# Optimization experiments

Hardware: AMD Instinct MI355X
Metric: run time of the kernel (lower is better)

## Reference

```python
import jax, jax.numpy as jnp
import numpy as np

B, L, H, W = 4, 16, 4096, 128   # W == nfeat == nclass (required by out.reshape)
NHID = 256

def setup_inputs() -> dict:
    key = jax.random.key(0)
    k1, k2, k3, k4 = jax.random.split(key, 4)
    x = jax.random.normal(k1, (B, L, H, W), dtype=jnp.float32)
    # row-normalized-ish dense adjacency stand-in for the sparse normalized adj
    adj = jax.random.uniform(k2, (H, H), dtype=jnp.float32) / H
    # GraphConvolution params: support = input @ Wk; out = adj @ support + bk
    W1 = jax.random.normal(k3, (W, NHID), dtype=jnp.float32) / np.sqrt(W)
    b1 = jnp.zeros((NHID,), dtype=jnp.float32)
    W2 = jax.random.normal(k4, (NHID, W), dtype=jnp.float32) / np.sqrt(NHID)
    b2 = jnp.zeros((W,), dtype=jnp.float32)
    return {"x": x, "adj": adj, "W1": W1, "b1": b1, "W2": W2, "b2": b2}

def reference(x, adj, W1, b1, W2, b2):
    Bv, Lv, Hv, Wv = x.shape
    xf = x.reshape(Bv * Lv, Hv, Wv)                      # [BL, H, F]
    # gc1: transform then aggregate, fused over all slices (replaces per-slice loop)
    h = jnp.einsum('nm,bmf->bnf', adj, xf @ W1) + b1     # [BL, H, nhid]
    h = jax.nn.relu(h)
    # dropout: inference mode (training=False) -> identity
    out = jnp.einsum('nm,bmf->bnf', adj, h @ W2) + b2    # [BL, H, nclass]
    out = out.reshape(Bv, Lv, Hv, Wv)
    return jax.nn.log_softmax(out, axis=-1)
```

## Files before the change

### kernel.cpp

```cpp
#include <hip/hip_runtime.h>

typedef __attribute__((ext_vector_type(4))) float f32x4;
typedef __attribute__((ext_vector_type(16))) float f32x16;
typedef __attribute__((ext_vector_type(4))) int i32x4;
typedef __attribute__((ext_vector_type(8))) int i32x8;
typedef union { i32x8 v8; i32x4 v4[2]; } opnd;

__device__ __forceinline__ unsigned fp4q(float v) {
  float a = __builtin_fabsf(v);
  unsigned q = (unsigned)(a > 0.25f) + (a > 0.75f) + (a > 1.25f) + (a > 1.75f)
             + (a > 2.5f) + (a > 3.5f) + (a > 5.0f);
  return q | (v < 0.0f ? 8u : 0u);
}

#if __has_builtin(__builtin_amdgcn_cvt_scalef32_pk_fp4_f32)
#define PKFP4(old, x, y, s) __builtin_amdgcn_cvt_scalef32_pk_fp4_f32((old), (x), (y), 1.0f, (s))
#else
#define PKFP4(old, x, y, s) ((old) | ((fp4q(x) | (fp4q(y) << 4)) << (8 * (s))))
#endif

__device__ __forceinline__ long tiled_addr(long r, long k, int nkb) {
  return (((r >> 5) * nkb) + (k >> 6)) * 2048 + ((k & 16) ? 1024 : 0)
       + (((r & 31) + (((k >> 5) & 1) << 5)) << 4) + (k & 15);
}
__device__ __forceinline__ long tile4_addr(long r, long k, int nkb) {
  return (((r >> 5) * nkb) + (k >> 6)) * 1024
       + (((r & 31) + (((k >> 5) & 1) << 5)) << 4) + ((k & 31) >> 1);
}

__device__ __forceinline__ long remap_wg(int lin, int nwg, int gx) {
  long g = lin;
  if ((nwg & 7) == 0) {
    int cpx = nwg >> 3;
    int gyx = cpx / gx;
    int xcd = lin & 7, idx = lin >> 3;
    if ((gx & 3) == 0 && gyx >= 4 && (gyx & 3) == 0) {
      int st = idx >> 4, wi = idx & 15;
      int nstr = gx >> 2;
      int str = st % nstr, stc = st / nstr;
      int r = str * 4 + (wi & 3);
      int c2 = stc * 4 + (wi >> 2);
      g = (long)xcd * cpx + (long)c2 * gx + r;
    } else {
      g = (long)xcd * cpx + idx;
    }
  }
  return g;
}

__global__ __launch_bounds__(256) void cvtAdj4t(const float* __restrict__ in,
                                                unsigned char* __restrict__ out, long n) {
  long i = ((long)blockIdx.x * 256 + threadIdx.x) * 8;
  if (i >= n) return;
  float4 a = *(const float4*)(in + i);
  float4 b = *(const float4*)(in + i + 4);
  const float S = 24576.0f;
  unsigned word = PKFP4(0u, a.x * S, a.y * S, 0);
  word = PKFP4(word, a.z * S, a.w * S, 1);
  word = PKFP4(word, b.x * S, b.y * S, 2);
  word = PKFP4(word, b.z * S, b.w * S, 3);
  long r = i >> 12;
  long k = i & 4095;
  *(int*)(out + tile4_addr(r, k, 64)) = (int)word;
}

__global__ __launch_bounds__(256) void cvtX4t(const float* __restrict__ X,
                                              unsigned char* __restrict__ out4) {
  __shared__ float tile[32][33];
  const int tid = threadIdx.x;
  const long bl = blockIdx.z;
  const int m0 = blockIdx.y * 32;
  const int w0 = blockIdx.x * 32;
  const float* xb = X + (bl * 4096 + m0) * 128 + w0;
  int row = tid >> 3, cg = tid & 7;
  float4 v = *(const float4*)(xb + (long)row * 128 + cg * 4);
  tile[row][cg * 4 + 0] = v.x;
  tile[row][cg * 4 + 1] = v.y;
  tile[row][cg * 4 + 2] = v.z;
  tile[row][cg * 4 + 3] = v.w;
  __syncthreads();
  if (tid < 128) {
    int wv = tid & 31, mg = tid >> 5;
    float t[8];
#pragma unroll
    for (int i = 0; i < 8; ++i) t[i] = tile[mg * 8 + i][wv];
    unsigned word = PKFP4(0u, t[0], t[1], 0);
    word = PKFP4(word, t[2], t[3], 1);
    word = PKFP4(word, t[4], t[5], 2);
    word = PKFP4(word, t[6], t[7], 3);
    long r = bl * 128 + w0 + wv;
    long k = m0 + mg * 8;
    *(int*)(out4 + tile4_addr(r, k, 64)) = (int)word;
  }
}

__global__ __launch_bounds__(256) void prep_params(const float* __restrict__ W1,
                                                   const float* __restrict__ W2,
                                                   unsigned char* __restrict__ W1T8,
                                                   unsigned char* __restrict__ W2T8) {
  int idx = blockIdx.x * 256 + threadIdx.x;
  if (idx < 32768) {
    int f = idx >> 7, wv = idx & 127;
    float v = W1[wv * 256 + f] * 16.0f;
    int pk = __builtin_amdgcn_cvt_pk_fp8_f32(v, v, 0, 0);
    W1T8[tiled_addr(f, wv, 2)] = (unsigned char)(pk & 0xff);
  } else {
    int t = idx - 32768;
    int cc = t >> 8, f = t & 255;
    float v = W2[f * 128 + cc] * 16.0f;
    int pk = __builtin_amdgcn_cvt_pk_fp8_f32(v, v, 0, 0);
    W2T8[tiled_addr(cc, f, 4)] = (unsigned char)(pk & 0xff);
  }
}

__global__ __launch_bounds__(256, 3) void gemmS1(const unsigned char* __restrict__ A4,
                                                 const unsigned char* __restrict__ X4,
                                                 const unsigned char* __restrict__ W1T8,
                                                 const unsigned char* __restrict__ W2T8,
                                                 unsigned char* __restrict__ t2T4,
                                                 const float* __restrict__ b1,
                                                 int K, int gx) {
  __shared__ unsigned char lds[49152];
  const int tid = threadIdx.x;
  const int l = tid & 63;
  const int w = tid >> 6;
  long g = remap_wg(blockIdx.x, gridDim.x, gx);
  const long row0 = (g % gx) * 128;
  const long bl = g / gx;
  const int nkb = K >> 6;
  const int wr = w >> 1, wc = w & 1;
  const unsigned char* sAp = A4 + (((row0 >> 5) + w) * (long)nkb) * 1024 + l * 16;
  const unsigned char* sXp = X4 + ((bl * 4 + w) * (long)nkb) * 1024 + l * 16;
  unsigned char* ldsw = lds + w * 1024;
  const unsigned char* rA = lds + (wr * 2) * 1024 + l * 16;
  const unsigned char* rX = lds + 4096 + (wc * 2) * 1024 + l * 16;

  f32x16 acc[2][2] = {};
  opnd aE[2], xE[2], aO[2], xO[2];
  const i32x4 z4 = {0, 0, 0, 0};
#pragma unroll
  for (int fi = 0; fi < 2; ++fi) {
    aE[fi].v4[1] = z4; xE[fi].v4[1] = z4;
    aO[fi].v4[1] = z4; xO[fi].v4[1] = z4;
  }

#define STG(B, SL) do { long o0_ = (long)(2 * (B)) * 1024; long o1_ = o0_ + 1024;     \
    unsigned char* d_ = ldsw + (SL) * 16384;                                          \
    __builtin_amdgcn_global_load_lds((const unsigned int*)(const void*)(sAp + o0_),   \
                                     (unsigned int*)(d_), 16, 0, 0);                  \
    __builtin_amdgcn_global_load_lds((const unsigned int*)(const void*)(sXp + o0_),   \
                                     (unsigned int*)(d_ + 4096), 16, 0, 0);           \
    __builtin_amdgcn_global_load_lds((const unsigned int*)(const void*)(sAp + o1_),   \
                                     (unsigned int*)(d_ + 8192), 16, 0, 0);           \
    __builtin_amdgcn_global_load_lds((const unsigned int*)(const void*)(sXp + o1_),   \
                                     (unsigned int*)(d_ + 12288), 16, 0, 0);          \
  } while (0)
#define LDF(SL, HALF, AV, XV) do { const long s_ = (SL) * 16384 + (HALF) * 8192;      \
    AV[0].v4[0] = *(const i32x4*)(rA + s_);                                           \
    AV[1].v4[0] = *(const i32x4*)(rA + s_ + 1024);                                    \
    XV[0].v4[0] = *(const i32x4*)(rX + s_);                                           \
    XV[1].v4[0] = *(const i32x4*)(rX + s_ + 1024); } while (0)
#define MFMAS(AV, XV) do {                                                            \
    __builtin_amdgcn_s_setprio(1);                                                    \
    _Pragma("unroll") for (int fi = 0; fi < 2; ++fi)                                  \
      _Pragma("unroll") for (int j = 0; j < 2; ++j)                                   \
        acc[fi][j] = __builtin_amdgcn_mfma_scale_f32_32x32x64_f8f6f4(                 \
            XV[j].v8, AV[fi].v8, acc[fi][j], 4, 4, 0, 127, 0, 124);                   \
    __builtin_amdgcn_s_setprio(0); } while (0)
#define BODY(SL, SS, DOSTG, B, N) do {                                                \
    LDF(SL, 0, aE, xE);                                                               \
    if (DOSTG) STG((B) + 2, SS);                                                      \
    LDF(SL, 1, aO, xO);                                                               \
    MFMAS(aE, xE);                                                                    \
    MFMAS(aO, xO);                                                                    \
    asm volatile("s_waitcnt vmcnt(" N ")" ::: "memory");                              \
    __builtin_amdgcn_s_barrier(); } while (0)

  STG(0, 0); STG(1, 1);
  asm volatile("s_waitcnt vmcnt(4)" ::: "memory");
  __builtin_amdgcn_s_barrier();
  for (int b = 0; b < 30; b += 3) {
    BODY(0, 2, 1, b + 0, "4");
    BODY(1, 0, 1, b + 1, "4");
    BODY(2, 1, 1, b + 2, "4");
  }
  BODY(0, 0, 0, 30, "0");
  BODY(1, 0, 0, 31, "0");
#undef STG
#undef LDF
#undef MFMAS
#undef BODY

  unsigned char* S1buf = lds;
  unsigned char* hbuf = lds + 16384;

  const int hi = l >> 5;
  const int ln = l & 31;
#pragma unroll
  for (int fi = 0; fi < 2; ++fi) {
    int n = (wr * 2 + fi) * 32 + ln;
#pragma unroll
    for (int j = 0; j < 2; ++j) {
      int wb = (wc * 2 + j) * 32 + 4 * hi;
#pragma unroll
      for (int r4 = 0; r4 < 4; ++r4) {
        int w0 = wb + 8 * r4;
        int word = __builtin_amdgcn_cvt_pk_fp8_f32(acc[fi][j][4 * r4 + 0],
                                                   acc[fi][j][4 * r4 + 1], 0, false);
        word = __builtin_amdgcn_cvt_pk_fp8_f32(acc[fi][j][4 * r4 + 2],
                                               acc[fi][j][4 * r4 + 3], word, true);
        *(int*)(S1buf + tiled_addr(n, w0, 2)) = word;
      }
    }
  }
  __syncthreads();

  const float c1 = 128.0f / 49152.0f;
#pragma unroll
  for (int hh = 0; hh < 2; ++hh) {
#pragma unroll
    for (int fi = 0; fi < 2; ++fi)
#pragma unroll
      for (int jb = 0; jb < 2; ++jb) acc[fi][jb] = (f32x16){};
#pragma unroll
    for (int kt1 = 0; kt1 < 2; ++kt1) {
#pragma unroll
      for (int jb = 0; jb < 2; ++jb) {
        opnd aw;
        const unsigned char* pW = W1T8 + (long)((hh * 4 + wc * 2 + jb) * 2 + kt1) * 2048 + l * 16;
        aw.v4[0] = *(const i32x4*)(pW);
        aw.v4[1] = *(const i32x4*)(pW + 1024);
#pragma unroll
        for (int fi = 0; fi < 2; ++fi) {
          opnd bs;
          const unsigned char* pS = S1buf + (long)((wr * 2 + fi) * 2 + kt1) * 2048 + l * 16;
          bs.v4[0] = *(const i32x4*)(pS);
          bs.v4[1] = *(const i32x4*)(pS + 1024);
          acc[fi][jb] = __builtin_amdgcn_mfma_scale_f32_32x32x64_f8f6f4(
              aw.v8, bs.v8, acc[fi][jb], 0, 0, 0, 127, 0, 127);
        }
      }
    }
#pragma unroll
    for (int jb = 0; jb < 2; ++jb) {
      int fb = (hh * 4 + wc * 2 + jb) * 32 + 4 * hi;
#pragma unroll
      for (int r4 = 0; r4 < 4; ++r4) {
        int f0 = fb + 8 * r4;
        float4 bb = *(const float4*)(b1 + f0);
#pragma unroll
        for (int fi = 0; fi < 2; ++fi) {
          int n = (wr * 2 + fi) * 32 + ln;
          float v0 = fmaxf(fmaf(acc[fi][jb][4 * r4 + 0], c1, bb.x * 128.0f), 0.0f);
          float v1 = fmaxf(fmaf(acc[fi][jb][4 * r4 + 1], c1, bb.y * 128.0f), 0.0f);
          float v2 = fmaxf(fmaf(acc[fi][jb][4 * r4 + 2], c1, bb.z * 128.0f), 0.0f);
          float v3 = fmaxf(fmaf(acc[fi][jb][4 * r4 + 3], c1, bb.w * 128.0f), 0.0f);
          int word = __builtin_amdgcn_cvt_pk_fp8_f32(v0, v1, 0, false);
          word = __builtin_amdgcn_cvt_pk_fp8_f32(v2, v3, word, true);
          *(int*)(hbuf + tiled_addr(n, f0, 4)) = word;
        }
      }
    }
  }
  __syncthreads();

#pragma unroll
  for (int fi = 0; fi < 2; ++fi)
#pragma unroll
    for (int jb = 0; jb < 2; ++jb) acc[fi][jb] = (f32x16){};
#pragma unroll
  for (int kt2 = 0; kt2 < 4; ++kt2) {
#pragma unroll
    for (int jb = 0; jb < 2; ++jb) {
      opnd bw;
      const unsigned char* pW = W2T8 + (long)((wc * 2 + jb) * 4 + kt2) * 2048 + l * 16;
      bw.v4[0] = *(const i32x4*)(pW);
      bw.v4[1] = *(const i32x4*)(pW + 1024);
#pragma unroll
      for (int fi = 0; fi < 2; ++fi) {
        opnd ah;
        const unsigned char* pH = hbuf + (long)((wr * 2 + fi) * 4 + kt2) * 2048 + l * 16;
        ah.v4[0] = *(const i32x4*)(pH);
        ah.v4[1] = *(const i32x4*)(pH + 1024);
        acc[fi][jb] = __builtin_amdgcn_mfma_scale_f32_32x32x64_f8f6f4(
            ah.v8, bw.v8, acc[fi][jb], 0, 0, 0, 127, 0, 127);
      }
    }
  }
  unsigned char* ob = t2T4 + bl * 262144;
#pragma unroll
  for (int fi = 0; fi < 2; ++fi) {
#pragma unroll
    for (int jb = 0; jb < 2; ++jb) {
      int cc = wc * 64 + jb * 32 + ln;
#pragma unroll
      for (int run = 0; run < 4; ++run) {
        long n0 = row0 + wr * 64 + fi * 32 + 8 * run + 4 * hi;
        const float s = 0.125f;
        unsigned pkw = PKFP4(0u, acc[fi][jb][run * 4 + 0] * s,
                                 acc[fi][jb][run * 4 + 1] * s, 0);
        pkw = PKFP4(pkw, acc[fi][jb][run * 4 + 2] * s,
                         acc[fi][jb][run * 4 + 3] * s, 1);
        *(ushort*)(ob + tile4_addr(cc, n0, 64)) = (ushort)pkw;
      }
    }
  }
}

__global__ __launch_bounds__(512) void gemm256sm(const unsigned char* __restrict__ A4,
                                                 const unsigned char* __restrict__ B4,
                                                 float* __restrict__ out,
                                                 const float* __restrict__ bias,
                                                 float ooScale, int K, int gx,
                                                 int chunkBase) {
  __shared__ unsigned char ring[65536];
  const int tid = threadIdx.x;
  const int l = tid & 63;
  const int w = tid >> 6;
  int lin = blockIdx.x;
  const int nwg = gridDim.x;
  if (gx == 16 && (nwg & 63) == 0) {
    int xcd = lin & 7, idx = lin >> 3;
    int cpg = nwg >> 6;
    int r = ((xcd & 1) << 3) + (idx & 7);
    int c = (xcd >> 1) * cpg + (idx >> 3);
    lin = c * gx + r;
  } else if ((nwg & 7) == 0) {
    int cpx = nwg >> 3;
    lin = (lin & 7) * cpx + (lin >> 3);
  }
  const long row0 = (long)(lin % gx) * 256;
  const long col0 = (long)(lin / gx) * 256;
  const int nkb = K >> 6;
  const unsigned char* sBp = B4 + (((col0 >> 5) + w) * (long)nkb) * 1024 + l * 16;
  unsigned char* ringw = ring + w * 1024;
  const unsigned char* ringr = ring + ((w & 1) * 4) * 1024 + l * 16;
  const unsigned char* pA = A4 + (((row0 + (w >> 1) * 64) >> 5) * (long)nkb) * 1024 + l * 16;

  f32x16 acc[2][4] = {};
  opnd bv[4], a0v[2], a1v[2], a2v[2], a3v[2];
  const i32x4 z4 = {0, 0, 0, 0};
#pragma unroll
  for (int j = 0; j < 4; ++j) bv[j].v4[1] = z4;
#pragma unroll
  for (int fi = 0; fi < 2; ++fi) {
    a0v[fi].v4[1] = z4; a1v[fi].v4[1] = z4; a2v[fi].v4[1] = z4; a3v[fi].v4[1] = z4;
  }

#define STGB(KT) __builtin_amdgcn_global_load_lds(                                    \
    (const unsigned int*)(const void*)(sBp + (long)(KT) * 1024),                      \
    (unsigned int*)(ringw + (((KT) & 7) << 13)), 16, 0, 0)
#define LOADA(KT, AV) do { long o_ = (long)(KT) * 1024;                               \
    AV[0].v4[0] = *(const i32x4*)(pA + o_);                                           \
    AV[1].v4[0] = *(const i32x4*)(pA + (long)nkb * 1024 + o_); } while (0)
#define LDB(KT) do { const unsigned char* p_ = ringr + (((KT) & 7) << 13);            \
    bv[0].v4[0] = *(const i32x4*)(p_);                                                \
    bv[1].v4[0] = *(const i32x4*)(p_ + 1024);                                         \
    bv[2].v4[0] = *(const i32x4*)(p_ + 2048);                                         \
    bv[3].v4[0] = *(const i32x4*)(p_ + 3072); } while (0)
#define MFMAS(AV) do { __builtin_amdgcn_s_setprio(1);                                 \
    _Pragma("unroll") for (int fi = 0; fi < 2; ++fi)                                  \
      _Pragma("unroll") for (int j = 0; j < 4; ++j)                                   \
        acc[fi][j] = __builtin_amdgcn_mfma_scale_f32_32x32x64_f8f6f4(                 \
            AV[fi].v8, bv[j].v8, acc[fi][j], 4, 4, 0, 127, 0, 127);                   \
    __builtin_amdgcn_s_setprio(0); } while (0)
#define BODY(KT, N, DOSTG, DOA, ALD, AUSE) do {                                       \
    LDB(KT);                                                                          \
    if (DOA) LOADA((KT) + 3, ALD);                                                    \
    if (DOSTG) STGB((KT) + 6);                                                        \
    asm volatile("s_waitcnt vmcnt(" N ")" ::: "memory");                              \
    MFMAS(AUSE);                                                                      \
    __builtin_amdgcn_s_barrier(); } while (0)

  const int nkt = K >> 6;
  LOADA(0, a0v); LOADA(1, a1v); LOADA(2, a2v);
  STGB(0); STGB(1); STGB(2); STGB(3); STGB(4); STGB(5);
  asm volatile("s_waitcnt vmcnt(5)" ::: "memory");
  __builtin_amdgcn_s_barrier();

  BODY(0, "7", 1, 1, a3v, a0v);
  BODY(1, "9", 1, 1, a0v, a1v);
  BODY(2, "11", 1, 1, a1v, a2v);
  for (int kt = 3; kt + 9 <= nkt - 1; kt += 4) {
    BODY(kt,     "10", 1, 1, a2v, a3v);
    BODY(kt + 1, "10", 1, 1, a3v, a0v);
    BODY(kt + 2, "10", 1, 1, a0v, a1v);
    BODY(kt + 3, "10", 1, 1, a1v, a2v);
  }
  BODY(55, "10", 1, 1, a2v, a3v);
  BODY(56, "10", 1, 1, a3v, a0v);
  BODY(57, "10", 1, 1, a0v, a1v);
  BODY(58, "9",  0, 1, a1v, a2v);
  BODY(59, "8",  0, 1, a2v, a3v);
  BODY(60, "7",  0, 1, a3v, a0v);
  BODY(61, "4",  0, 0, a0v, a1v);
  BODY(62, "2",  0, 0, a0v, a2v);
  BODY(63, "0",  0, 0, a0v, a3v);
#undef STGB
#undef LOADA
#undef LDB
#undef MFMAS
#undef BODY

  const int hi = l >> 5;
  const int bl = (int)(col0 >> 7) + (w & 1);
  float bb[4];
#pragma unroll
  for (int j = 0; j < 4; ++j) bb[j] = bias[j * 32 + (l & 31)];
#pragma unroll
  for (int fi = 0; fi < 2; ++fi) {
#pragma unroll
    for (int rr = 0; rr < 16; ++rr) {
      float v0 = acc[fi][0][rr] * ooScale + bb[0];
      float v1 = acc[fi][1][rr] * ooScale + bb[1];
      float v2 = acc[fi][2][rr] * ooScale + bb[2];
      float v3 = acc[fi][3][rr] * ooScale + bb[3];
      float m = fmaxf(fmaxf(v0, v1), fmaxf(v2, v3));
#pragma unroll
      for (int o = 16; o > 0; o >>= 1) m = fmaxf(m, __shfl_xor(m, o));
      float s = __expf(v0 - m) + __expf(v1 - m) + __expf(v2 - m) + __expf(v3 - m);
#pragma unroll
      for (int o = 16; o > 0; o >>= 1) s += __shfl_xor(s, o);
      float lse = m + __logf(s);
      long row = row0 + (w >> 1) * 64 + fi * 32 + ((rr & 3) + 8 * (rr >> 2) + 4 * hi);
      float* dst = out + ((long)(chunkBase + bl) * 4096 + row) * 128;
      dst[(l & 31)] = v0 - lse;
      dst[32 + (l & 31)] = v1 - lse;
      dst[64 + (l & 31)] = v2 - lse;
      dst[96 + (l & 31)] = v3 - lse;
    }
  }
}

extern "C" void kernel_launch(void* const* d_in, const int* in_sizes, int n_in,
                              void* d_out, int out_size, void* d_ws, size_t ws_size,
                              hipStream_t stream) {
  const float* x = (const float*)d_in[0];
  const float* adj = (const float*)d_in[1];
  const float* W1 = (const float*)d_in[2];
  const float* b1 = (const float*)d_in[3];
  const float* W2 = (const float*)d_in[4];
  const float* b2 = (const float*)d_in[5];
  float* out = (float*)d_out;
  char* ws = (char*)d_ws;

  unsigned char* adj4 = (unsigned char*)ws;
  unsigned char* W1T8 = (unsigned char*)(ws + 8388608);
  unsigned char* W2T8 = (unsigned char*)(ws + 8388608 + 32768);
  const size_t base = 9ull * 1024 * 1024;

  const int cands[6] = {64, 32, 16, 8, 4, 2};
  int c = 2;
  for (int t = 0; t < 6; ++t) {
    size_t need = base + (size_t)cands[t] * 524288;
    if (need <= ws_size) { c = cands[t]; break; }
  }
  unsigned char* x4T = (unsigned char*)(ws + base);
  unsigned char* t2T4 = x4T + (size_t)c * 262144;

  cvtAdj4t<<<8192, 256, 0, stream>>>(adj, adj4, (long)4096 * 4096);
  prep_params<<<256, 256, 0, stream>>>(W1, W2, W1T8, W2T8);

  int chunks = 64 / c;
  for (int cb = 0; cb < chunks; ++cb) {
    int base_bl = cb * c;
    const float* xc = x + (long)base_bl * 4096 * 128;

    cvtX4t<<<dim3(4, 128, c), 256, 0, stream>>>(xc, x4T);
    gemmS1<<<32 * c, 256, 0, stream>>>(adj4, x4T, W1T8, W2T8, t2T4, b1, 4096, 32);
    gemm256sm<<<16 * (c / 2), 512, 0, stream>>>(adj4, t2T4, out, b2,
                                                1.0f / 6291456.0f, 4096, 16, base_bl);
  }
}
```

Before: 229.9 us.

## Split MFMA loop bodies into ping-pong phases with barrier-synced LDS loads

Both GEMM main loops are split into two half-phases. Each phase issues its LDS fragment loads, meets a workgroup barrier, waits on lgkmcnt, and then runs half of the MFMAs behind a sched_barrier. The aim is to interleave waves so memory and matrix work alternate across the workgroup, ping-pong style. The second kernel's vmcnt thresholds are loosened so more global loads stay in flight. The cost is extra barriers per iteration, and the hand-tuned vmcnt counts carry a correctness risk if they are miscounted.

```diff
diff --git a/kernel.cpp b/kernel.cpp
--- a/kernel.cpp
+++ b/kernel.cpp
@@ -167,29 +167,40 @@
         acc[fi][j] = __builtin_amdgcn_mfma_scale_f32_32x32x64_f8f6f4(                 \
             XV[j].v8, AV[fi].v8, acc[fi][j], 4, 4, 0, 127, 0, 124);                   \
     __builtin_amdgcn_s_setprio(0); } while (0)
-#define BODY(SL, SS, DOSTG, B, N) do {                                                \
+#define PH1S(SL, SS, DOSTG, B) do {                                                   \
     LDF(SL, 0, aE, xE);                                                               \
     if (DOSTG) STG((B) + 2, SS);                                                      \
+    __builtin_amdgcn_s_barrier();                                                     \
+    asm volatile("s_waitcnt lgkmcnt(0)" ::: "memory");                                \
+    __builtin_amdgcn_sched_barrier(0);                                                \
+    MFMAS(aE, xE);                                                                    \
+    __builtin_amdgcn_s_barrier(); } while (0)
+#define PH2S(SL, N) do {                                                              \
     LDF(SL, 1, aO, xO);                                                               \
-    MFMAS(aE, xE);                                                                    \
+    __builtin_amdgcn_s_barrier();                                                     \
+    asm volatile("s_waitcnt lgkmcnt(0)" ::: "memory");                                \
+    __builtin_amdgcn_sched_barrier(0);                                                \
     MFMAS(aO, xO);                                                                    \
     asm volatile("s_waitcnt vmcnt(" N ")" ::: "memory");                              \
     __builtin_amdgcn_s_barrier(); } while (0)
+#define BODYS(SL, SS, DOSTG, B, N) do { PH1S(SL, SS, DOSTG, B); PH2S(SL, N); } while (0)
 
   STG(0, 0); STG(1, 1);
   asm volatile("s_waitcnt vmcnt(4)" ::: "memory");
   __builtin_amdgcn_s_barrier();
   for (int b = 0; b < 30; b += 3) {
-    BODY(0, 2, 1, b + 0, "4");
-    BODY(1, 0, 1, b + 1, "4");
-    BODY(2, 1, 1, b + 2, "4");
-  }
-  BODY(0, 0, 0, 30, "0");
-  BODY(1, 0, 0, 31, "0");
+    BODYS(0, 2, 1, b + 0, "4");
+    BODYS(1, 0, 1, b + 1, "4");
+    BODYS(2, 1, 1, b + 2, "4");
+  }
+  BODYS(0, 0, 0, 30, "0");
+  BODYS(1, 0, 0, 31, "0");
 #undef STG
 #undef LDF
 #undef MFMAS
-#undef BODY
+#undef PH1S
+#undef PH2S
+#undef BODYS
 
   unsigned char* S1buf = lds;
   unsigned char* hbuf = lds + 16384;
@@ -353,23 +364,39 @@
 #define LOADA(KT, AV) do { long o_ = (long)(KT) * 1024;                               \
     AV[0].v4[0] = *(const i32x4*)(pA + o_);                                           \
     AV[1].v4[0] = *(const i32x4*)(pA + (long)nkb * 1024 + o_); } while (0)
-#define LDB(KT) do { const unsigned char* p_ = ringr + (((KT) & 7) << 13);            \
+#define LDB01(KT) do { const unsigned char* p_ = ringr + (((KT) & 7) << 13);          \
     bv[0].v4[0] = *(const i32x4*)(p_);                                                \
-    bv[1].v4[0] = *(const i32x4*)(p_ + 1024);                                         \
+    bv[1].v4[0] = *(const i32x4*)(p_ + 1024); } while (0)
+#define LDB23(KT) do { const unsigned char* p_ = ringr + (((KT) & 7) << 13);          \
     bv[2].v4[0] = *(const i32x4*)(p_ + 2048);                                         \
     bv[3].v4[0] = *(const i32x4*)(p_ + 3072); } while (0)
-#define MFMAS(AV) do { __builtin_amdgcn_s_setprio(1);                                 \
+#define MFMA01(AV) do { __builtin_amdgcn_s_setprio(1);                                \
     _Pragma("unroll") for (int fi = 0; fi < 2; ++fi)                                  \
-      _Pragma("unroll") for (int j = 0; j < 4; ++j)                                   \
+      _Pragma("unroll") for (int j = 0; j < 2; ++j)                                   \
+        acc[fi][j] = __builtin_amdgcn_mfma_scale_f32_32x32x64_f8f6f4(                 \
+            AV[fi].v8, bv[j].v8, acc[fi][j], 4, 4, 0, 127, 0, 127);                   \
+    __builtin_amdgcn_s_setprio(0); } while (0)
+#define MFMA23(AV) do { __builtin_amdgcn_s_setprio(1);                                \
+    _Pragma("unroll") for (int fi = 0; fi < 2; ++fi)                                  \
+      _Pragma("unroll") for (int j = 2; j < 4; ++j)                                   \
         acc[fi][j] = __builtin_amdgcn_mfma_scale_f32_32x32x64_f8f6f4(                 \
             AV[fi].v8, bv[j].v8, acc[fi][j], 4, 4, 0, 127, 0, 127);                   \
     __builtin_amdgcn_s_setprio(0); } while (0)
 #define BODY(KT, N, DOSTG, DOA, ALD, AUSE) do {                                       \
-    LDB(KT);                                                                          \
+    LDB01(KT);                                                                        \
+    if (DOSTG) STGB((KT) + 6);                                                        \
+    __builtin_amdgcn_s_barrier();                                                     \
+    asm volatile("s_waitcnt lgkmcnt(0)" ::: "memory");                                \
+    __builtin_amdgcn_sched_barrier(0);                                                \
+    MFMA01(AUSE);                                                                     \
+    __builtin_amdgcn_s_barrier();                                                     \
+    LDB23(KT);                                                                        \
     if (DOA) LOADA((KT) + 3, ALD);                                                    \
-    if (DOSTG) STGB((KT) + 6);                                                        \
+    __builtin_amdgcn_s_barrier();                                                     \
+    asm volatile("s_waitcnt lgkmcnt(0)" ::: "memory");                                \
+    __builtin_amdgcn_sched_barrier(0);                                                \
+    MFMA23(AUSE);                                                                     \
     asm volatile("s_waitcnt vmcnt(" N ")" ::: "memory");                              \
-    MFMAS(AUSE);                                                                      \
     __builtin_amdgcn_s_barrier(); } while (0)
 
   const int nkt = K >> 6;
@@ -378,28 +405,34 @@
   asm volatile("s_waitcnt vmcnt(5)" ::: "memory");
   __builtin_amdgcn_s_barrier();
 
-  BODY(0, "7", 1, 1, a3v, a0v);
-  BODY(1, "9", 1, 1, a0v, a1v);
+  BODY(0, "7",  1, 1, a3v, a0v);
+  BODY(1, "9",  1, 1, a0v, a1v);
   BODY(2, "11", 1, 1, a1v, a2v);
-  for (int kt = 3; kt + 9 <= nkt - 1; kt += 4) {
-    BODY(kt,     "10", 1, 1, a2v, a3v);
-    BODY(kt + 1, "10", 1, 1, a3v, a0v);
-    BODY(kt + 2, "10", 1, 1, a0v, a1v);
-    BODY(kt + 3, "10", 1, 1, a1v, a2v);
-  }
-  BODY(55, "10", 1, 1, a2v, a3v);
-  BODY(56, "10", 1, 1, a3v, a0v);
-  BODY(57, "10", 1, 1, a0v, a1v);
-  BODY(58, "9",  0, 1, a1v, a2v);
-  BODY(59, "8",  0, 1, a2v, a3v);
-  BODY(60, "7",  0, 1, a3v, a0v);
-  BODY(61, "4",  0, 0, a0v, a1v);
-  BODY(62, "2",  0, 0, a0v, a2v);
+  BODY(3, "13", 1, 1, a2v, a3v);
+  BODY(4, "15", 1, 1, a3v, a0v);
+  for (int kt = 5; kt <= 49; kt += 4) {
+    BODY(kt,     "17", 1, 1, a0v, a1v);
+    BODY(kt + 1, "17", 1, 1, a1v, a2v);
+    BODY(kt + 2, "17", 1, 1, a2v, a3v);
+    BODY(kt + 3, "17", 1, 1, a3v, a0v);
+  }
+  BODY(53, "17", 1, 1, a0v, a1v);
+  BODY(54, "17", 1, 1, a1v, a2v);
+  BODY(55, "17", 1, 1, a2v, a3v);
+  BODY(56, "17", 1, 1, a3v, a0v);
+  BODY(57, "17", 1, 1, a0v, a1v);
+  BODY(58, "16", 0, 1, a1v, a2v);
+  BODY(59, "15", 0, 1, a2v, a3v);
+  BODY(60, "14", 0, 1, a3v, a0v);
+  BODY(61, "11", 0, 0, a0v, a1v);
+  BODY(62, "8",  0, 0, a0v, a2v);
   BODY(63, "0",  0, 0, a0v, a3v);
 #undef STGB
 #undef LOADA
-#undef LDB
-#undef MFMAS
+#undef LDB01
+#undef LDB23
+#undef MFMA01
+#undef MFMA23
 #undef BODY
 
   const int hi = l >> 5;
```

Result: no change. 233.1 us (+1.4%).

## Retile second adjacency GEMM into 128-row, 256-thread blocks with shared staging pipeline

Applied to the files above, without the earlier changes.

Replaces the 256x256, 512-thread second-stage GEMM with a 128-row x one-slice tile using 256 threads. It reuses the triple-buffered LDS staging scheme from the first GEMM, which loads both A and B via global_load_lds. The launch grid changes to 32 blocks per slice with occupancy hint of 3 blocks per CU. This aims at more parallelism and a simpler pipeline, at the cost of less operand reuse per block and more total adjacency traffic.

```diff
diff --git a/kernel.cpp b/kernel.cpp
--- a/kernel.cpp
+++ b/kernel.cpp
@@ -167,7 +167,7 @@
         acc[fi][j] = __builtin_amdgcn_mfma_scale_f32_32x32x64_f8f6f4(                 \
             XV[j].v8, AV[fi].v8, acc[fi][j], 4, 4, 0, 127, 0, 124);                   \
     __builtin_amdgcn_s_setprio(0); } while (0)
-#define BODY(SL, SS, DOSTG, B, N) do {                                                \
+#define BODYS(SL, SS, DOSTG, B, N) do {                                               \
     LDF(SL, 0, aE, xE);                                                               \
     if (DOSTG) STG((B) + 2, SS);                                                      \
     LDF(SL, 1, aO, xO);                                                               \
@@ -180,16 +180,16 @@
   asm volatile("s_waitcnt vmcnt(4)" ::: "memory");
   __builtin_amdgcn_s_barrier();
   for (int b = 0; b < 30; b += 3) {
-    BODY(0, 2, 1, b + 0, "4");
-    BODY(1, 0, 1, b + 1, "4");
-    BODY(2, 1, 1, b + 2, "4");
-  }
-  BODY(0, 0, 0, 30, "0");
-  BODY(1, 0, 0, 31, "0");
+    BODYS(0, 2, 1, b + 0, "4");
+    BODYS(1, 0, 1, b + 1, "4");
+    BODYS(2, 1, 1, b + 2, "4");
+  }
+  BODYS(0, 0, 0, 30, "0");
+  BODYS(1, 0, 0, 31, "0");
 #undef STG
 #undef LDF
 #undef MFMAS
-#undef BODY
+#undef BODYS
 
   unsigned char* S1buf = lds;
   unsigned char* hbuf = lds + 16384;
@@ -307,128 +307,103 @@
   }
 }
 
-__global__ __launch_bounds__(512) void gemm256sm(const unsigned char* __restrict__ A4,
-                                                 const unsigned char* __restrict__ B4,
-                                                 float* __restrict__ out,
-                                                 const float* __restrict__ bias,
-                                                 float ooScale, int K, int gx,
-                                                 int chunkBase) {
-  __shared__ unsigned char ring[65536];
+__global__ __launch_bounds__(256, 3) void gemm256sm(const unsigned char* __restrict__ A4,
+                                                    const unsigned char* __restrict__ B4,
+                                                    float* __restrict__ out,
+                                                    const float* __restrict__ bias,
+                                                    float ooScale, int K, int gx,
+                                                    int chunkBase) {
+  __shared__ unsigned char lds[49152];
   const int tid = threadIdx.x;
   const int l = tid & 63;
   const int w = tid >> 6;
-  int lin = blockIdx.x;
-  const int nwg = gridDim.x;
-  if (gx == 16 && (nwg & 63) == 0) {
-    int xcd = lin & 7, idx = lin >> 3;
-    int cpg = nwg >> 6;
-    int r = ((xcd & 1) << 3) + (idx & 7);
-    int c = (xcd >> 1) * cpg + (idx >> 3);
-    lin = c * gx + r;
-  } else if ((nwg & 7) == 0) {
-    int cpx = nwg >> 3;
-    lin = (lin & 7) * cpx + (lin >> 3);
-  }
-  const long row0 = (long)(lin % gx) * 256;
-  const long col0 = (long)(lin / gx) * 256;
+  long g = remap_wg(blockIdx.x, gridDim.x, gx);
+  const long row0 = (g % gx) * 128;
+  const long bl = g / gx;
   const int nkb = K >> 6;
-  const unsigned char* sBp = B4 + (((col0 >> 5) + w) * (long)nkb) * 1024 + l * 16;
-  unsigned char* ringw = ring + w * 1024;
-  const unsigned char* ringr = ring + ((w & 1) * 4) * 1024 + l * 16;
-  const unsigned char* pA = A4 + (((row0 + (w >> 1) * 64) >> 5) * (long)nkb) * 1024 + l * 16;
-
-  f32x16 acc[2][4] = {};
-  opnd bv[4], a0v[2], a1v[2], a2v[2], a3v[2];
+  const unsigned char* sAp = A4 + (((row0 >> 5) + w) * (long)nkb) * 1024 + l * 16;
+  const unsigned char* sXp = B4 + ((bl * 4 + w) * (long)nkb) * 1024 + l * 16;
+  unsigned char* ldsw = lds + w * 1024;
+  const unsigned char* rA = lds + w * 1024 + l * 16;
+  const unsigned char* rB = lds + 4096 + l * 16;
+
+  f32x16 acc[4] = {};
+  opnd aE, aO, bE[4], bO[4];
   const i32x4 z4 = {0, 0, 0, 0};
-#pragma unroll
-  for (int j = 0; j < 4; ++j) bv[j].v4[1] = z4;
-#pragma unroll
-  for (int fi = 0; fi < 2; ++fi) {
-    a0v[fi].v4[1] = z4; a1v[fi].v4[1] = z4; a2v[fi].v4[1] = z4; a3v[fi].v4[1] = z4;
-  }
-
-#define STGB(KT) __builtin_amdgcn_global_load_lds(                                    \
-    (const unsigned int*)(const void*)(sBp + (long)(KT) * 1024),                      \
-    (unsigned int*)(ringw + (((KT) & 7) << 13)), 16, 0, 0)
-#define LOADA(KT, AV) do { long o_ = (long)(KT) * 1024;                               \
-    AV[0].v4[0] = *(const i32x4*)(pA + o_);                                           \
-    AV[1].v4[0] = *(const i32x4*)(pA + (long)nkb * 1024 + o_); } while (0)
-#define LDB(KT) do { const unsigned char* p_ = ringr + (((KT) & 7) << 13);            \
-    bv[0].v4[0] = *(const i32x4*)(p_);                                                \
-    bv[1].v4[0] = *(const i32x4*)(p_ + 1024);                                         \
-    bv[2].v4[0] = *(const i32x4*)(p_ + 2048);                                         \
-    bv[3].v4[0] = *(const i32x4*)(p_ + 3072); } while (0)
-#define MFMAS(AV) do { __builtin_amdgcn_s_setprio(1);                                 \
-    _Pragma("unroll") for (int fi = 0; fi < 2; ++fi)                                  \
-      _Pragma("unroll") for (int j = 0; j < 4; ++j)                                   \
-        acc[fi][j] = __builtin_amdgcn_mfma_scale_f32_32x32x64_f8f6f4(                 \
-            AV[fi].v8, bv[j].v8, acc[fi][j], 4, 4, 0, 127, 0, 127);                   \
+  aE.v4[1] = z4; aO.v4[1] = z4;
+#pragma unroll
+  for (int j = 0; j < 4; ++j) { bE[j].v4[1] = z4; bO[j].v4[1] = z4; }
+
+#define STG(B, SL) do { long o0_ = (long)(2 * (B)) * 1024; long o1_ = o0_ + 1024;     \
+    unsigned char* d_ = ldsw + (SL) * 16384;                                          \
+    __builtin_amdgcn_global_load_lds((const unsigned int*)(const void*)(sAp + o0_),   \
+                                     (unsigned int*)(d_), 16, 0, 0);                  \
+    __builtin_amdgcn_global_load_lds((const unsigned int*)(const void*)(sXp + o0_),   \
+                                     (unsigned int*)(d_ + 4096), 16, 0, 0);           \
+    __builtin_amdgcn_global_load_lds((const unsigned int*)(const void*)(sAp + o1_),   \
+                                     (unsigned int*)(d_ + 8192), 16, 0, 0);           \
+    __builtin_amdgcn_global_load_lds((const unsigned int*)(const void*)(sXp + o1_),   \
+                                     (unsigned int*)(d_ + 12288), 16, 0, 0);          \
+  } while (0)
+#define LDF(SL, HALF, AV, BV) do { const long s_ = (SL) * 16384 + (HALF) * 8192;      \
+    AV.v4[0] = *(const i32x4*)(rA + s_);                                              \
+    BV[0].v4[0] = *(const i32x4*)(rB + s_);                                           \
+    BV[1].v4[0] = *(const i32x4*)(rB + s_ + 1024);                                    \
+    BV[2].v4[0] = *(const i32x4*)(rB + s_ + 2048);                                    \
+    BV[3].v4[0] = *(const i32x4*)(rB + s_ + 3072); } while (0)
+#define MFMAS(AV, BV) do {                                                            \
+    __builtin_amdgcn_s_setprio(1);                                                    \
+    _Pragma("unroll") for (int j = 0; j < 4; ++j)                                     \
+      acc[j] = __builtin_amdgcn_mfma_scale_f32_32x32x64_f8f6f4(                       \
+          AV.v8, BV[j].v8, acc[j], 4, 4, 0, 127, 0, 127);                             \
     __builtin_amdgcn_s_setprio(0); } while (0)
-#define BODY(KT, N, DOSTG, DOA, ALD, AUSE) do {                                       \
-    LDB(KT);                                                                          \
-    if (DOA) LOADA((KT) + 3, ALD);                                                    \
-    if (DOSTG) STGB((KT) + 6);                                                        \
+#define BODYS(SL, SS, DOSTG, B, N) do {                                               \
+    LDF(SL, 0, aE, bE);                                                               \
+    if (DOSTG) STG((B) + 2, SS);                                                      \
+    LDF(SL, 1, aO, bO);                                                               \
+    MFMAS(aE, bE);                                                                    \
+    MFMAS(aO, bO);                                                                    \
     asm volatile("s_waitcnt vmcnt(" N ")" ::: "memory");                              \
-    MFMAS(AUSE);                                                                      \
     __builtin_amdgcn_s_barrier(); } while (0)
 
-  const int nkt = K >> 6;
-  LOADA(0, a0v); LOADA(1, a1v); LOADA(2, a2v);
-  STGB(0); STGB(1); STGB(2); STGB(3); STGB(4); STGB(5);
-  asm volatile("s_waitcnt vmcnt(5)" ::: "memory");
+  STG(0, 0); STG(1, 1);
+  asm volatile("s_waitcnt vmcnt(4)" ::: "memory");
   __builtin_amdgcn_s_barrier();
-
-  BODY(0, "7", 1, 1, a3v, a0v);
-  BODY(1, "9", 1, 1, a0v, a1v);
-  BODY(2, "11", 1, 1, a1v, a2v);
-  for (int kt = 3; kt + 9 <= nkt - 1; kt += 4) {
-    BODY(kt,     "10", 1, 1, a2v, a3v);
-    BODY(kt + 1, "10", 1, 1, a3v, a0v);
-    BODY(kt + 2, "10", 1, 1, a0v, a1v);
-    BODY(kt + 3, "10", 1, 1, a1v, a2v);
-  }
-  BODY(55, "10", 1, 1, a2v, a3v);
-  BODY(56, "10", 1, 1, a3v, a0v);
-  BODY(57, "10", 1, 1, a0v, a1v);
-  BODY(58, "9",  0, 1, a1v, a2v);
-  BODY(59, "8",  0, 1, a2v, a3v);
-  BODY(60, "7",  0, 1, a3v, a0v);
-  BODY(61, "4",  0, 0, a0v, a1v);
-  BODY(62, "2",  0, 0, a0v, a2v);
-  BODY(63, "0",  0, 0, a0v, a3v);
-#undef STGB
-#undef LOADA
-#undef LDB
+  for (int b = 0; b < 30; b += 3) {
+    BODYS(0, 2, 1, b + 0, "4");
+    BODYS(1, 0, 1, b + 1, "4");
+    BODYS(2, 1, 1, b + 2, "4");
+  }
+  BODYS(0, 0, 0, 30, "0");
+  BODYS(1, 0, 0, 31, "0");
+#undef STG
+#undef LDF
 #undef MFMAS
-#undef BODY
+#undef BODYS
 
   const int hi = l >> 5;
-  const int bl = (int)(col0 >> 7) + (w & 1);
   float bb[4];
 #pragma unroll
   for (int j = 0; j < 4; ++j) bb[j] = bias[j * 32 + (l & 31)];
 #pragma unroll
-  for (int fi = 0; fi < 2; ++fi) {
-#pragma unroll
-    for (int rr = 0; rr < 16; ++rr) {
-      float v0 = acc[fi][0][rr] * ooScale + bb[0];
-      float v1 = acc[fi][1][rr] * ooScale + bb[1];
-      float v2 = acc[fi][2][rr] * ooScale + bb[2];
-      float v3 = acc[fi][3][rr] * ooScale + bb[3];
-      float m = fmaxf(fmaxf(v0, v1), fmaxf(v2, v3));
-#pragma unroll
-      for (int o = 16; o > 0; o >>= 1) m = fmaxf(m, __shfl_xor(m, o));
-      float s = __expf(v0 - m) + __expf(v1 - m) + __expf(v2 - m) + __expf(v3 - m);
-#pragma unroll
-      for (int o = 16; o > 0; o >>= 1) s += __shfl_xor(s, o);
-      float lse = m + __logf(s);
-      long row = row0 + (w >> 1) * 64 + fi * 32 + ((rr & 3) + 8 * (rr >> 2) + 4 * hi);
-      float* dst = out + ((long)(chunkBase + bl) * 4096 + row) * 128;
-      dst[(l & 31)] = v0 - lse;
-      dst[32 + (l & 31)] = v1 - lse;
-      dst[64 + (l & 31)] = v2 - lse;
-      dst[96 + (l & 31)] = v3 - lse;
-    }
+  for (int rr = 0; rr < 16; ++rr) {
+    float v0 = acc[0][rr] * ooScale + bb[0];
+    float v1 = acc[1][rr] * ooScale + bb[1];
+    float v2 = acc[2][rr] * ooScale + bb[2];
+    float v3 = acc[3][rr] * ooScale + bb[3];
+    float m = fmaxf(fmaxf(v0, v1), fmaxf(v2, v3));
+#pragma unroll
+    for (int o = 16; o > 0; o >>= 1) m = fmaxf(m, __shfl_xor(m, o));
+    float s = __expf(v0 - m) + __expf(v1 - m) + __expf(v2 - m) + __expf(v3 - m);
+#pragma unroll
+    for (int o = 16; o > 0; o >>= 1) s += __shfl_xor(s, o);
+    float lse = m + __logf(s);
+    long row = row0 + w * 32 + ((rr & 3) + 8 * (rr >> 2) + 4 * hi);
+    float* dst = out + ((long)(chunkBase + bl) * 4096 + row) * 128;
+    dst[(l & 31)] = v0 - lse;
+    dst[32 + (l & 31)] = v1 - lse;
+    dst[64 + (l & 31)] = v2 - lse;
+    dst[96 + (l & 31)] = v3 - lse;
   }
 }
 
@@ -468,7 +443,7 @@
 
     cvtX4t<<<dim3(4, 128, c), 256, 0, stream>>>(xc, x4T);
     gemmS1<<<32 * c, 256, 0, stream>>>(adj4, x4T, W1T8, W2T8, t2T4, b1, 4096, 32);
-    gemm256sm<<<16 * (c / 2), 512, 0, stream>>>(adj4, t2T4, out, b2,
-                                                1.0f / 6291456.0f, 4096, 16, base_bl);
-  }
-}
+    gemm256sm<<<32 * c, 256, 0, stream>>>(adj4, t2T4, out, b2,
+                                          1.0f / 6291456.0f, 4096, 32, base_bl);
+  }
+}
```

Measured after the change: 236.2 us. 1.03x slower.

## Load A operand directly to registers and deepen X LDS pipeline in gemmS1

Applied to the files above, without the earlier changes.

The main GEMM loop of gemmS1 stops staging the adjacency (A) tile through LDS. Each wave now reads its A fragments straight from global memory into a three-deep register rotation. Only the X operand still goes through LDS, now in a four-slot ring with one 64-wide k step per iteration instead of two. This cuts LDS traffic and LDS footprint for A, at the cost of more VGPRs, more barriers per k, and A global loads that are no longer shared across the two column waves.

```diff
diff --git a/kernel.cpp b/kernel.cpp
--- a/kernel.cpp
+++ b/kernel.cpp
@@ -129,65 +129,68 @@
   const long bl = g / gx;
   const int nkb = K >> 6;
   const int wr = w >> 1, wc = w & 1;
-  const unsigned char* sAp = A4 + (((row0 >> 5) + w) * (long)nkb) * 1024 + l * 16;
   const unsigned char* sXp = X4 + ((bl * 4 + w) * (long)nkb) * 1024 + l * 16;
   unsigned char* ldsw = lds + w * 1024;
-  const unsigned char* rA = lds + (wr * 2) * 1024 + l * 16;
-  const unsigned char* rX = lds + 4096 + (wc * 2) * 1024 + l * 16;
+  const unsigned char* rX = lds + (wc * 2) * 1024 + l * 16;
+  const unsigned char* pA = A4 + (((row0 >> 5) + wr * 2) * (long)nkb) * 1024 + l * 16;
 
   f32x16 acc[2][2] = {};
-  opnd aE[2], xE[2], aO[2], xO[2];
+  opnd xv[2], a0[2], a1[2], a2[2];
   const i32x4 z4 = {0, 0, 0, 0};
-#pragma unroll
-  for (int fi = 0; fi < 2; ++fi) {
-    aE[fi].v4[1] = z4; xE[fi].v4[1] = z4;
-    aO[fi].v4[1] = z4; xO[fi].v4[1] = z4;
-  }
-
-#define STG(B, SL) do { long o0_ = (long)(2 * (B)) * 1024; long o1_ = o0_ + 1024;     \
-    unsigned char* d_ = ldsw + (SL) * 16384;                                          \
-    __builtin_amdgcn_global_load_lds((const unsigned int*)(const void*)(sAp + o0_),   \
-                                     (unsigned int*)(d_), 16, 0, 0);                  \
-    __builtin_amdgcn_global_load_lds((const unsigned int*)(const void*)(sXp + o0_),   \
-                                     (unsigned int*)(d_ + 4096), 16, 0, 0);           \
-    __builtin_amdgcn_global_load_lds((const unsigned int*)(const void*)(sAp + o1_),   \
-                                     (unsigned int*)(d_ + 8192), 16, 0, 0);           \
-    __builtin_amdgcn_global_load_lds((const unsigned int*)(const void*)(sXp + o1_),   \
-                                     (unsigned int*)(d_ + 12288), 16, 0, 0);          \
-  } while (0)
-#define LDF(SL, HALF, AV, XV) do { const long s_ = (SL) * 16384 + (HALF) * 8192;      \
-    AV[0].v4[0] = *(const i32x4*)(rA + s_);                                           \
-    AV[1].v4[0] = *(const i32x4*)(rA + s_ + 1024);                                    \
-    XV[0].v4[0] = *(const i32x4*)(rX + s_);                                           \
-    XV[1].v4[0] = *(const i32x4*)(rX + s_ + 1024); } while (0)
-#define MFMAS(AV, XV) do {                                                            \
+  xv[0].v4[1] = z4; xv[1].v4[1] = z4;
+#pragma unroll
+  for (int fi = 0; fi < 2; ++fi) { a0[fi].v4[1] = z4; a1[fi].v4[1] = z4; a2[fi].v4[1] = z4; }
+
+#define STGX(KT, SL) __builtin_amdgcn_global_load_lds(                                \
+    (const unsigned int*)(const void*)(sXp + (long)(KT) * 1024),                      \
+    (unsigned int*)(ldsw + (SL) * 4096), 16, 0, 0)
+#define LOADA(KT, AV) do { long o_ = (long)(KT) * 1024;                               \
+    AV[0].v4[0] = *(const i32x4*)(pA + o_);                                           \
+    AV[1].v4[0] = *(const i32x4*)(pA + (long)nkb * 1024 + o_); } while (0)
+#define LDX(SL) do { const unsigned char* p_ = rX + (SL) * 4096;                      \
+    xv[0].v4[0] = *(const i32x4*)(p_);                                                \
+    xv[1].v4[0] = *(const i32x4*)(p_ + 1024); } while (0)
+#define MFMAS(AV) do {                                                                \
     __builtin_amdgcn_s_setprio(1);                                                    \
     _Pragma("unroll") for (int fi = 0; fi < 2; ++fi)                                  \
       _Pragma("unroll") for (int j = 0; j < 2; ++j)                                   \
         acc[fi][j] = __builtin_amdgcn_mfma_scale_f32_32x32x64_f8f6f4(                 \
-            XV[j].v8, AV[fi].v8, acc[fi][j], 4, 4, 0, 127, 0, 124);                   \
+            xv[j].v8, AV[fi].v8, acc[fi][j], 4, 4, 0, 127, 0, 124);                   \
     __builtin_amdgcn_s_setprio(0); } while (0)
-#define BODY(SL, SS, DOSTG, B, N) do {                                                \
-    LDF(SL, 0, aE, xE);                                                               \
-    if (DOSTG) STG((B) + 2, SS);                                                      \
-    LDF(SL, 1, aO, xO);                                                               \
-    MFMAS(aE, xE);                                                                    \
-    MFMAS(aO, xO);                                                                    \
+#define BODY(KT, SLR, SLS, AUSE, ALD, N, DOSTG, DOA) do {                             \
+    LDX(SLR);                                                                         \
+    if (DOSTG) STGX((KT) + 3, SLS);                                                   \
+    if (DOA) LOADA((KT) + 2, ALD);                                                    \
     asm volatile("s_waitcnt vmcnt(" N ")" ::: "memory");                              \
+    MFMAS(AUSE);                                                                      \
     __builtin_amdgcn_s_barrier(); } while (0)
 
-  STG(0, 0); STG(1, 1);
-  asm volatile("s_waitcnt vmcnt(4)" ::: "memory");
+  STGX(0, 0); STGX(1, 1); STGX(2, 2);
+  LOADA(0, a0); LOADA(1, a1);
+  asm volatile("s_waitcnt vmcnt(6)" ::: "memory");
   __builtin_amdgcn_s_barrier();
-  for (int b = 0; b < 30; b += 3) {
-    BODY(0, 2, 1, b + 0, "4");
-    BODY(1, 0, 1, b + 1, "4");
-    BODY(2, 1, 1, b + 2, "4");
-  }
-  BODY(0, 0, 0, 30, "0");
-  BODY(1, 0, 0, 31, "0");
-#undef STG
-#undef LDF
+
+  BODY(0, 0, 3, a0, a2, "5", 1, 1);
+  for (int b = 1; b <= 49; b += 12) {
+    BODY(b + 0,  1, 0, a1, a0, "6", 1, 1);
+    BODY(b + 1,  2, 1, a2, a1, "6", 1, 1);
+    BODY(b + 2,  3, 2, a0, a2, "6", 1, 1);
+    BODY(b + 3,  0, 3, a1, a0, "6", 1, 1);
+    BODY(b + 4,  1, 0, a2, a1, "6", 1, 1);
+    BODY(b + 5,  2, 1, a0, a2, "6", 1, 1);
+    BODY(b + 6,  3, 2, a1, a0, "6", 1, 1);
+    BODY(b + 7,  0, 3, a2, a1, "6", 1, 1);
+    BODY(b + 8,  1, 0, a0, a2, "6", 1, 1);
+    BODY(b + 9,  2, 1, a1, a0, "6", 1, 1);
+    BODY(b + 10, 3, 2, a2, a1, "6", 1, 1);
+    BODY(b + 11, 0, 3, a0, a2, "6", 1, 1);
+  }
+  BODY(61, 1, 0, a1, a0, "5", 0, 1);
+  BODY(62, 2, 0, a2, a0, "2", 0, 0);
+  BODY(63, 3, 0, a0, a0, "0", 0, 0);
+#undef STGX
+#undef LOADA
+#undef LDX
 #undef MFMAS
 #undef BODY
 
```

New measurement: 230.0 us. No clear change (+0.1%).
